# Kernel tuning notes

Hardware: AMD Instinct MI355X
Metric: run time of the kernel (lower is better)

The kernel has to match this reference:

```python
import jax, jax.numpy as jnp
import numpy as np

PARAM_BOUNDS = {'R': (1e-4, 0.2), 'C': (1e5, 1e8), 'A_eff': (0.0, 0.2), 'hvac_gain': (1.0, 2e4)}
PARAM_INIT = {'R': 0.007, 'C': 3.5e6, 'A_eff': 0.01, 'hvac_gain': 450.0}
DELTA_T = 900.0  # seconds per step (from args.delta_t)
COOLING_SIGN = -1.0  # mode == 'cool'


def _raw_init(name):
    lo, hi = PARAM_BOUNDS[name]
    p = (PARAM_INIT[name] - lo) / (hi - lo)
    return np.float32(np.log(p / (1.0 - p)))  # logit


def _bounded(raw, lo, hi):
    return lo + (hi - lo) * jax.nn.sigmoid(raw)


def setup_inputs() -> dict:
    key = jax.random.key(0)
    B, S = 8192, 4096
    input_vec = jax.random.normal(key, (B, S, 4), dtype=jnp.float32)
    return {
        'input_vec': input_vec,
        'raw_R': jnp.asarray(_raw_init('R')),
        'raw_C': jnp.asarray(_raw_init('C')),
        'raw_A_eff': jnp.asarray(_raw_init('A_eff')),
        'raw_hvac_gain': jnp.asarray(_raw_init('hvac_gain')),
    }


def reference(input_vec, raw_R, raw_C, raw_A_eff, raw_hvac_gain):
    R = _bounded(raw_R, *PARAM_BOUNDS['R'])
    C = _bounded(raw_C, *PARAM_BOUNDS['C'])
    A_eff = _bounded(raw_A_eff, *PARAM_BOUNDS['A_eff'])
    g = _bounded(raw_hvac_gain, *PARAM_BOUNDS['hvac_gain'])

    t_in = input_vec[:, :, 0]   # (B, S)
    t_out = input_vec[:, :, 1]
    hvac_u = input_vec[:, :, 2]
    solar = input_vec[:, :, 3]

    def step(t_prev, x):
        to, u, so = x
        heat = (to - t_prev) / R
        hvac = COOLING_SIGN * g * u
        sol = A_eff * so
        t_next = t_prev + DELTA_T * (heat + hvac + sol) / C
        return t_next, t_next

    t0 = t_in[:, 0]  # initial indoor temperature, (B,)
    xs = (t_out.T, hvac_u.T, solar.T)  # time-major (S, B)
    _, preds = jax.lax.scan(step, t0, xs)  # preds: (S, B)
    return jnp.transpose(preds)[..., None]  # (B, S, 1)
```

## Files before the change

kernel.cpp:

```cpp
#include <hip/hip_runtime.h>
#include <math.h>


#define SLEN 4096
#define THREADS 256
#define PER 16
#define PAD_IDX(s) ((((s) >> 4) * 17) + ((s) & 15))

__global__ __launch_bounds__(THREADS) void rc_scan_kernel(
    const float* __restrict__ in,
    const float* __restrict__ rawR,
    const float* __restrict__ rawC,
    const float* __restrict__ rawA,
    const float* __restrict__ rawG,
    float* __restrict__ out)
{
    __shared__ float sm_c[256 * 17];
    __shared__ float sm_m[THREADS];
    __shared__ float sm_d[THREADS];

    const int row = blockIdx.x;
    const int tid = threadIdx.x;

    const float sR = 1.0f / (1.0f + expf(-rawR[0]));
    const float sC = 1.0f / (1.0f + expf(-rawC[0]));
    const float sA = 1.0f / (1.0f + expf(-rawA[0]));
    const float sG = 1.0f / (1.0f + expf(-rawG[0]));
    const float R = 0.0001f + (0.2f - 0.0001f) * sR;
    const float C = 100000.0f + (100000000.0f - 100000.0f) * sC;
    const float A = 0.2f * sA;
    const float g = 1.0f + (20000.0f - 1.0f) * sG;

    const float k     = 900.0f / C;
    const float kinvR = k / R;
    const float a     = 1.0f - kinvR;
    const float kg    = k * g;
    const float kA    = k * A;

    const float4* rowp = (const float4*)(in + (size_t)row * (size_t)SLEN * 4);

    const float t0 = rowp[0].x;

#pragma unroll
    for (int q = 0; q < PER; ++q) {
        const int s = tid + THREADS * q;
        float4 v = rowp[s];
        sm_c[PAD_IDX(s)] = kinvR * v.y - kg * v.z + kA * v.w;
    }
    __syncthreads();

    float c[PER];
#pragma unroll
    for (int j = 0; j < PER; ++j) c[j] = sm_c[tid * 17 + j];

    float d = 0.0f;
#pragma unroll
    for (int j = 0; j < PER; ++j) d = fmaf(a, d, c[j]);
    const float a2 = a * a, a4 = a2 * a2, a8 = a4 * a4;
    const float m16 = a8 * a8;

    float cm = m16, cd = d;
    sm_m[tid] = cm;
    sm_d[tid] = cd;
    __syncthreads();
    for (int off = 1; off < THREADS; off <<= 1) {
        float pm = 1.0f, pd = 0.0f;
        const bool has = (tid >= off);
        if (has) { pm = sm_m[tid - off]; pd = sm_d[tid - off]; }
        __syncthreads();
        if (has) { cd = fmaf(cm, pd, cd); cm = pm * cm; }
        sm_m[tid] = cm;
        sm_d[tid] = cd;
        __syncthreads();
    }

    float t;
    if (tid == 0) t = t0;
    else          t = fmaf(sm_m[tid - 1], t0, sm_d[tid - 1]);

#pragma unroll
    for (int j = 0; j < PER; ++j) {
        t = fmaf(a, t, c[j]);
        sm_c[tid * 17 + j] = t;
    }
    __syncthreads();

    float* orow = out + (size_t)row * SLEN;
#pragma unroll
    for (int q = 0; q < 4; ++q) {
        const int s0 = q * 1024 + 4 * tid;
        float4 v;
        v.x = sm_c[PAD_IDX(s0 + 0)];
        v.y = sm_c[PAD_IDX(s0 + 1)];
        v.z = sm_c[PAD_IDX(s0 + 2)];
        v.w = sm_c[PAD_IDX(s0 + 3)];
        *(float4*)(orow + s0) = v;
    }
}

extern "C" void kernel_launch(void* const* d_in, const int* in_sizes, int n_in,
                              void* d_out, int out_size, void* d_ws, size_t ws_size,
                              hipStream_t stream) {
    const float* in   = (const float*)d_in[0];
    const float* rawR = (const float*)d_in[1];
    const float* rawC = (const float*)d_in[2];
    const float* rawA = (const float*)d_in[3];
    const float* rawG = (const float*)d_in[4];
    float* out = (float*)d_out;

    const int B = in_sizes[0] / (SLEN * 4);
    rc_scan_kernel<<<dim3(B), dim3(THREADS), 0, stream>>>(
        in, rawR, rawC, rawA, rawG, out);
}
```

Baseline: 721.9 us.

## Replace block-wide shared-memory scan with wavefront shuffle scan plus cross-wave carry

Replaces the 8-step Hillis-Steele scan over shared memory, which needed two barriers per step, with a 64-lane __shfl_up scan inside each wavefront. A small shared array then carries results across the four wavefronts, so only one barrier remains. Each lane builds its decay prefix from powers of a^16, and the per-thread register array is dropped by reading chunk values straight from LDS twice. Launch bounds now request 8 blocks per CU to raise occupancy, which caps registers per thread.

After: 731.2 us. No clear change (+1.3%).

```diff
diff --git a/kernel.cpp b/kernel.cpp
--- a/kernel.cpp
+++ b/kernel.cpp
@@ -5,9 +5,8 @@
 #define SLEN 4096
 #define THREADS 256
 #define PER 16
-#define PAD_IDX(s) ((((s) >> 4) * 17) + ((s) & 15))
 
-__global__ __launch_bounds__(THREADS) void rc_scan_kernel(
+__global__ __launch_bounds__(THREADS, 8) void rc_scan_kernel(
     const float* __restrict__ in,
     const float* __restrict__ rawR,
     const float* __restrict__ rawC,
@@ -16,11 +15,12 @@
     float* __restrict__ out)
 {
     __shared__ float sm_c[256 * 17];
-    __shared__ float sm_m[THREADS];
-    __shared__ float sm_d[THREADS];
+    __shared__ float sm_w[4];
 
-    const int row = blockIdx.x;
-    const int tid = threadIdx.x;
+    const int row  = blockIdx.x;
+    const int tid  = threadIdx.x;
+    const int lane = tid & 63;
+    const int wid  = tid >> 6;
 
     const float sR = 1.0f / (1.0f + expf(-rawR[0]));
     const float sC = 1.0f / (1.0f + expf(-rawC[0]));
@@ -37,51 +37,56 @@
     const float kg    = k * g;
     const float kA    = k * A;
 
-    const float4* rowp = (const float4*)(in + (size_t)row * (size_t)SLEN * 4);
+    const float4* rowp = (const float4*)(in + (size_t)row * (size_t)(SLEN * 4));
 
-    const float t0 = rowp[0].x;
+    const float t0 = in[(size_t)row * (size_t)(SLEN * 4)];
 
+    const int sbase = (tid >> 4) * 17 + (tid & 15);
 #pragma unroll
     for (int q = 0; q < PER; ++q) {
-        const int s = tid + THREADS * q;
-        float4 v = rowp[s];
-        sm_c[PAD_IDX(s)] = kinvR * v.y - kg * v.z + kA * v.w;
+        float4 v = rowp[tid + THREADS * q];
+        sm_c[sbase + 272 * q] = kinvR * v.y - kg * v.z + kA * v.w;
     }
     __syncthreads();
 
-    float c[PER];
-#pragma unroll
-    for (int j = 0; j < PER; ++j) c[j] = sm_c[tid * 17 + j];
-
+    const int cbase = tid * 17;
     float d = 0.0f;
 #pragma unroll
-    for (int j = 0; j < PER; ++j) d = fmaf(a, d, c[j]);
+    for (int j = 0; j < PER; ++j) d = fmaf(a, d, sm_c[cbase + j]);
+
     const float a2 = a * a, a4 = a2 * a2, a8 = a4 * a4;
     const float m16 = a8 * a8;
 
-    float cm = m16, cd = d;
-    sm_m[tid] = cm;
-    sm_d[tid] = cd;
-    __syncthreads();
-    for (int off = 1; off < THREADS; off <<= 1) {
-        float pm = 1.0f, pd = 0.0f;
-        const bool has = (tid >= off);
-        if (has) { pm = sm_m[tid - off]; pd = sm_d[tid - off]; }
-        __syncthreads();
-        if (has) { cd = fmaf(cm, pd, cd); cm = pm * cm; }
-        sm_m[tid] = cm;
-        sm_d[tid] = cd;
-        __syncthreads();
+    float M = m16;
+#pragma unroll
+    for (int off = 1; off < 64; off <<= 1) {
+        float od = __shfl_up(d, off, 64);
+        if (lane >= off) d = fmaf(M, od, d);
+        M *= M;
     }
 
-    float t;
-    if (tid == 0) t = t0;
-    else          t = fmaf(sm_m[tid - 1], t0, sm_d[tid - 1]);
+    if (lane == 63) sm_w[wid] = d;
+    __syncthreads();
+
+    float E = t0;
+    for (int v = 0; v < wid; ++v) E = fmaf(M, E, sm_w[v]);
+
+    float dx = __shfl_up(d, 1, 64);
+    if (lane == 0) dx = 0.0f;
+
+    float alpha = 1.0f, b = m16;
+#pragma unroll
+    for (int kk = 0; kk < 6; ++kk) {
+        if (lane & (1 << kk)) alpha *= b;
+        b *= b;
+    }
+
+    float t = fmaf(alpha, E, dx);
 
 #pragma unroll
     for (int j = 0; j < PER; ++j) {
-        t = fmaf(a, t, c[j]);
-        sm_c[tid * 17 + j] = t;
+        t = fmaf(a, t, sm_c[cbase + j]);
+        sm_c[cbase + j] = t;
     }
     __syncthreads();
 
@@ -89,11 +94,12 @@
 #pragma unroll
     for (int q = 0; q < 4; ++q) {
         const int s0 = q * 1024 + 4 * tid;
+        const int p  = ((s0 >> 4) * 17) + (s0 & 15);
         float4 v;
-        v.x = sm_c[PAD_IDX(s0 + 0)];
-        v.y = sm_c[PAD_IDX(s0 + 1)];
-        v.z = sm_c[PAD_IDX(s0 + 2)];
-        v.w = sm_c[PAD_IDX(s0 + 3)];
+        v.x = sm_c[p + 0];
+        v.y = sm_c[p + 1];
+        v.z = sm_c[p + 2];
+        v.w = sm_c[p + 3];
         *(float4*)(orow + s0) = v;
     }
 }
```
